# Kernel tuning notes

Measured on AMD Instinct MI355X. Metric: run time of the kernel, lower is better.

## Reference

```python
import jax, jax.numpy as jnp
import numpy as np

N = 100000   # nodes
E = 1000000  # directed edges
C = 64       # channels
K = 4        # propagation hops
DT = 1.0     # dt; exp_init=False branch: 2*x + dt^2*conv(x) - x_pre


def setup_inputs() -> dict:
    key = jax.random.key(0)
    k1, k2, k3, k4, k5 = jax.random.split(key, 5)
    x = jax.random.normal(k1, (N, C), dtype=jnp.float32)
    x_pre = jax.random.normal(k2, (N, C), dtype=jnp.float32)
    edge_index = jax.random.randint(k3, (2, E), 0, N, dtype=jnp.int32)
    bound = 1.0 / np.sqrt(C)  # PyG Linear default (kaiming-uniform-like)
    W = jax.random.uniform(k4, (C, C), jnp.float32, -bound, bound)
    b = jax.random.uniform(k5, (C,), jnp.float32, -bound, bound)
    return {"x": x, "x_pre": x_pre, "edge_index": edge_index, "W": W, "b": b}


def _sgc(x, edge_index, W, b):
    # gcn_norm: add self-loops, symmetric normalization D^-1/2 (A+I) D^-1/2
    loop = jnp.arange(N, dtype=edge_index.dtype)
    src = jnp.concatenate([edge_index[0], loop])  # source j
    dst = jnp.concatenate([edge_index[1], loop])  # target i
    deg = jax.ops.segment_sum(jnp.ones(src.shape, jnp.float32), dst, num_segments=N)
    dinv = jnp.where(deg > 0, jax.lax.rsqrt(deg), 0.0)
    norm = dinv[src] * dinv[dst]  # [E+N]
    h = x
    for _ in range(K):  # K-hop sparse propagation (gather -> scale -> scatter-add)
        h = jax.ops.segment_sum(h[src] * norm[:, None], dst, num_segments=N)
    return h @ W.T + b  # SGConv final linear


def reference(x, x_pre, edge_index, W, b):
    return 2.0 * x + (DT * DT) * _sgc(x, edge_index, W, b) - x_pre
```

## Files before the change

### kernel.cpp

```cpp
#include <hip/hip_runtime.h>
#include <hip/hip_fp16.h>

#define CCH 64
#define NBLK 128
#define BKT  256


__global__ void countA(const int* __restrict__ dst, int* __restrict__ cntmat,
                       int E, int chunk, int B) {
    __shared__ int h[512];
    int t = threadIdx.x, blk = blockIdx.x;
    for (int i = t; i < B; i += 256) h[i] = 0;
    __syncthreads();
    int e0 = blk * chunk, e1 = min(e0 + chunk, E);
    for (int e = e0 + t; e < e1; e += 256) atomicAdd(&h[dst[e] >> 8], 1);
    __syncthreads();
    for (int i = t; i < B; i += 256) cntmat[i * NBLK + blk] = h[i];
}

__global__ void scan1(const int* __restrict__ cnt, int* __restrict__ part,
                      int* __restrict__ bsum, int N) {
    __shared__ int s[256];
    int t = threadIdx.x;
    int base = blockIdx.x * 1024 + t * 4;
    int v0 = (base + 0 < N) ? cnt[base + 0] : 0;
    int v1 = (base + 1 < N) ? cnt[base + 1] : 0;
    int v2 = (base + 2 < N) ? cnt[base + 2] : 0;
    int v3 = (base + 3 < N) ? cnt[base + 3] : 0;
    s[t] = v0 + v1 + v2 + v3;
    __syncthreads();
    for (int off = 1; off < 256; off <<= 1) {
        int xx = (t >= off) ? s[t - off] : 0;
        __syncthreads();
        s[t] += xx;
        __syncthreads();
    }
    int excl = (t == 0) ? 0 : s[t - 1];
    if (t == 255) bsum[blockIdx.x] = s[255];
    if (base + 0 < N) part[base + 0] = excl;
    if (base + 1 < N) part[base + 1] = excl + v0;
    if (base + 2 < N) part[base + 2] = excl + v0 + v1;
    if (base + 3 < N) part[base + 3] = excl + v0 + v1 + v2;
}

__global__ void scan2(int* __restrict__ bsum, int NB) {
    __shared__ int s[256];
    int t = threadIdx.x;
    int base = t * 4;
    int v0 = (base + 0 < NB) ? bsum[base + 0] : 0;
    int v1 = (base + 1 < NB) ? bsum[base + 1] : 0;
    int v2 = (base + 2 < NB) ? bsum[base + 2] : 0;
    int v3 = (base + 3 < NB) ? bsum[base + 3] : 0;
    s[t] = v0 + v1 + v2 + v3;
    __syncthreads();
    for (int off = 1; off < 256; off <<= 1) {
        int xx = (t >= off) ? s[t - off] : 0;
        __syncthreads();
        s[t] += xx;
        __syncthreads();
    }
    int excl = (t == 0) ? 0 : s[t - 1];
    if (base + 0 < NB) bsum[base + 0] = excl;
    if (base + 1 < NB) bsum[base + 1] = excl + v0;
    if (base + 2 < NB) bsum[base + 2] = excl + v0 + v1;
    if (base + 3 < NB) bsum[base + 3] = excl + v0 + v1 + v2;
}

__global__ void partA(const int* __restrict__ src, const int* __restrict__ dst,
                      const int* __restrict__ part, const int* __restrict__ bsum,
                      unsigned* __restrict__ brec, int E, int chunk, int B) {
    __shared__ int cur[512];
    int t = threadIdx.x, blk = blockIdx.x;
    for (int i = t; i < B; i += 256) {
        int idx = i * NBLK + blk;
        cur[i] = part[idx] + bsum[idx >> 10];
    }
    __syncthreads();
    int e0 = blk * chunk, e1 = min(e0 + chunk, E);
    for (int e = e0 + t; e < e1; e += 256) {
        int s = src[e], d = dst[e];
        int pos = atomicAdd(&cur[d >> 8], 1);
        brec[pos] = ((unsigned)s << 8) | (unsigned)(d & 255);
    }
}

__global__ void buildB(const unsigned* __restrict__ brec, const int* __restrict__ part,
                       const int* __restrict__ bsum, int* __restrict__ row_ptr,
                       int* __restrict__ adj, float* __restrict__ dinv,
                       float* __restrict__ dinv2, const float* __restrict__ x,
                       __half* __restrict__ xh, int N, int B, int E) {
    __shared__ int hist[256];
    __shared__ int scanbuf[256];
    __shared__ int cursor[256];
    __shared__ float sdinv[256];
    int t = threadIdx.x, k = blockIdx.x;
    int i0 = k * NBLK;
    int base = part[i0] + bsum[i0 >> 10];
    int nextb;
    if (k + 1 < B) {
        int i1 = (k + 1) * NBLK;
        nextb = part[i1] + bsum[i1 >> 10];
    } else {
        nextb = E;
    }
    hist[t] = 0;
    __syncthreads();
    for (int i = base + t; i < nextb; i += 256) atomicAdd(&hist[brec[i] & 255u], 1);
    __syncthreads();
    int v = hist[t];
    scanbuf[t] = v;
    __syncthreads();
    for (int o = 1; o < 256; o <<= 1) {
        int xx = (t >= o) ? scanbuf[t - o] : 0;
        __syncthreads();
        scanbuf[t] += xx;
        __syncthreads();
    }
    int excl = scanbuf[t] - v;
    int node = k * 256 + t;
    float di = 0.f;
    if (node < N) {
        int p = base + excl;
        row_ptr[node] = p;
        cursor[t] = p;
        float dp1 = (float)v + 1.0f;
        di = rsqrtf(dp1);
        dinv[node]  = di;
        dinv2[node] = 1.0f / dp1;
    }
    sdinv[t] = di;
    if (k == 0 && t == 0) row_ptr[N] = E;
    __syncthreads();
    for (int i = base + t; i < nextb; i += 256) {
        unsigned r = brec[i];
        int pos = atomicAdd(&cursor[r & 255u], 1);
        adj[pos] = (int)(r >> 8);
    }
    int nodeBase = k * 256;
    for (int i = t; i < 2048; i += 256) {
        int nl = i >> 3;
        int node2 = nodeBase + nl;
        if (node2 < N) {
            float d = sdinv[nl];
            size_t baseE = (size_t)node2 * 64 + (size_t)(i & 7) * 8;
            float4 a = *(const float4*)&x[baseE];
            float4 c = *(const float4*)&x[baseE + 4];
            float4 o;
            __half2* op = (__half2*)&o;
            op[0] = __float22half2_rn(make_float2(d * a.x, d * a.y));
            op[1] = __float22half2_rn(make_float2(d * a.z, d * a.w));
            op[2] = __float22half2_rn(make_float2(d * c.x, d * c.y));
            op[3] = __float22half2_rn(make_float2(d * c.z, d * c.w));
            *(float4*)&xh[baseE] = o;
        }
    }
}


__device__ __forceinline__ void acc16w(float4 hv, float w, float* acc) {
    __half2* hp = (__half2*)&hv;
    #pragma unroll
    for (int i2 = 0; i2 < 4; ++i2) {
        float2 f = __half22float2(hp[i2]);
        acc[2 * i2]     = fmaf(w, f.x, acc[2 * i2]);
        acc[2 * i2 + 1] = fmaf(w, f.y, acc[2 * i2 + 1]);
    }
}

__global__ void __launch_bounds__(256, 6)
prop_kernel(const __half* __restrict__ hin, __half* __restrict__ hout,
            const int* __restrict__ row_ptr, const int* __restrict__ adj,
            const float* __restrict__ scale, int N) {
    int wid = (blockIdx.x * blockDim.x + threadIdx.x) >> 6;
    int nA = wid * 2;
    if (nA >= N) return;
    int nB = nA + 1;
    bool hasB = nB < N;
    int lane = threadIdx.x & 63;
    int grp  = lane >> 3;
    int q    = lane & 7;
    const float4* hin16 = (const float4*)hin;

    int rp0 = row_ptr[nA];
    int rp1 = row_ptr[nA + 1];
    int rp2 = hasB ? row_ptr[nA + 2] : rp1;
    int begA = rp0, cntA = rp1 - rp0;
    int begB = rp1, cntB = rp2 - rp1;
    int edA = adj[begA + lane];
    int edB = adj[begB + lane];
    float scA = scale[nA];
    float scB = hasB ? scale[nB] : 0.f;

    int selfn = (grp == 0) ? nA : ((grp == 1 && hasB) ? nB : 0);
    float4 selfv = hin16[(size_t)selfn * 8 + q];
    int nitA = cntA < 64 ? cntA : 64;
    int nitB = cntB < 64 ? cntB : 64;
    int jA0 = __shfl(edA, grp, 64);
    int jB0 = __shfl(edB, grp, 64);
    float4 pfA = hin16[(size_t)((grp < nitA) ? jA0 : 0) * 8 + q];
    float4 pfB = hin16[(size_t)((grp < nitB) ? jB0 : 0) * 8 + q];

    float accA[8] = {0.f, 0.f, 0.f, 0.f, 0.f, 0.f, 0.f, 0.f};
    float accB[8] = {0.f, 0.f, 0.f, 0.f, 0.f, 0.f, 0.f, 0.f};
    if (grp == 0)              acc16w(selfv, 1.f, accA);
    else if (grp == 1 && hasB) acc16w(selfv, 1.f, accB);

    int RA = (nitA + 7) >> 3;
    int RB = (nitB + 7) >> 3;
    int R  = RA > RB ? RA : RB;
    for (int r = 0; r < R; ++r) {
        float4 cA = pfA, cB = pfB;
        float wA = (r * 8 + grp < nitA) ? 1.f : 0.f;
        float wB = (r * 8 + grp < nitB) ? 1.f : 0.f;
        if (r + 1 < R) {
            int t1 = (r + 1) * 8 + grp;
            int jA = __shfl(edA, t1, 64);
            int jB = __shfl(edB, t1, 64);
            pfA = hin16[(size_t)((t1 < nitA) ? jA : 0) * 8 + q];
            pfB = hin16[(size_t)((t1 < nitB) ? jB : 0) * 8 + q];
        }
        acc16w(cA, wA, accA);
        acc16w(cB, wB, accB);
    }
    for (int e = begA + 64 + grp; e < begA + cntA; e += 8)
        acc16w(hin16[(size_t)adj[e] * 8 + q], 1.f, accA);
    for (int e = begB + 64 + grp; e < begB + cntB; e += 8)
        acc16w(hin16[(size_t)adj[e] * 8 + q], 1.f, accB);

    #pragma unroll
    for (int i = 0; i < 8; ++i) {
        accA[i] += __shfl_xor(accA[i], 8, 64);
        accA[i] += __shfl_xor(accA[i], 16, 64);
        accA[i] += __shfl_xor(accA[i], 32, 64);
        accB[i] += __shfl_xor(accB[i], 8, 64);
        accB[i] += __shfl_xor(accB[i], 16, 64);
        accB[i] += __shfl_xor(accB[i], 32, 64);
    }
    if (grp == 0 || (grp == 1 && hasB)) {
        int   row = (grp == 0) ? nA : nB;
        float sc  = (grp == 0) ? scA : scB;
        float v0 = (grp == 0) ? accA[0] : accB[0];
        float v1 = (grp == 0) ? accA[1] : accB[1];
        float v2 = (grp == 0) ? accA[2] : accB[2];
        float v3 = (grp == 0) ? accA[3] : accB[3];
        float v4 = (grp == 0) ? accA[4] : accB[4];
        float v5 = (grp == 0) ? accA[5] : accB[5];
        float v6 = (grp == 0) ? accA[6] : accB[6];
        float v7 = (grp == 0) ? accA[7] : accB[7];
        float4 o;
        __half2* op = (__half2*)&o;
        op[0] = __float22half2_rn(make_float2(sc * v0, sc * v1));
        op[1] = __float22half2_rn(make_float2(sc * v2, sc * v3));
        op[2] = __float22half2_rn(make_float2(sc * v4, sc * v5));
        op[3] = __float22half2_rn(make_float2(sc * v6, sc * v7));
        ((float4*)hout)[(size_t)row * 8 + q] = o;
    }
}

__global__ void __launch_bounds__(256, 2)
final_kernel(const __half* __restrict__ h, const float* __restrict__ x,
             const float* __restrict__ xp, const float* __restrict__ W,
             const float* __restrict__ b, float* __restrict__ out, int N) {
    __shared__ __align__(16) float ht[64 * 68];
    __shared__ __align__(16) float Wt[64 * 68];
    int t = threadIdx.x;
    int nodeBase = blockIdx.x * 64;

    for (int i = t; i < 1024; i += 256) {
        int c  = i >> 4;
        int k4 = i & 15;
        float4 w4 = ((const float4*)W)[i];
        Wt[(k4 * 4 + 0) * 68 + c] = w4.x;
        Wt[(k4 * 4 + 1) * 68 + c] = w4.y;
        Wt[(k4 * 4 + 2) * 68 + c] = w4.z;
        Wt[(k4 * 4 + 3) * 68 + c] = w4.w;
    }
    for (int i = t; i < 512; i += 256) {
        int n  = i >> 3;
        int k8 = i & 7;
        int node = nodeBase + n;
        float4 hv = (node < N) ? ((const float4*)h)[node * 8 + k8]
                               : make_float4(0.f, 0.f, 0.f, 0.f);
        __half2* hp = (__half2*)&hv;
        #pragma unroll
        for (int j = 0; j < 4; ++j) {
            float2 f = __half22float2(hp[j]);
            ht[(k8 * 8 + 2 * j)     * 68 + n] = f.x;
            ht[(k8 * 8 + 2 * j + 1) * 68 + n] = f.y;
        }
    }
    __syncthreads();

    int r0 = (t >> 4) * 4;
    int c0 = (t & 15) * 4;
    float acc[4][4] = {};
    #pragma unroll 8
    for (int k = 0; k < 64; ++k) {
        float4 hv = *(const float4*)&ht[k * 68 + r0];
        float4 wv = *(const float4*)&Wt[k * 68 + c0];
        acc[0][0] = fmaf(hv.x, wv.x, acc[0][0]);
        acc[0][1] = fmaf(hv.x, wv.y, acc[0][1]);
        acc[0][2] = fmaf(hv.x, wv.z, acc[0][2]);
        acc[0][3] = fmaf(hv.x, wv.w, acc[0][3]);
        acc[1][0] = fmaf(hv.y, wv.x, acc[1][0]);
        acc[1][1] = fmaf(hv.y, wv.y, acc[1][1]);
        acc[1][2] = fmaf(hv.y, wv.z, acc[1][2]);
        acc[1][3] = fmaf(hv.y, wv.w, acc[1][3]);
        acc[2][0] = fmaf(hv.z, wv.x, acc[2][0]);
        acc[2][1] = fmaf(hv.z, wv.y, acc[2][1]);
        acc[2][2] = fmaf(hv.z, wv.z, acc[2][2]);
        acc[2][3] = fmaf(hv.z, wv.w, acc[2][3]);
        acc[3][0] = fmaf(hv.w, wv.x, acc[3][0]);
        acc[3][1] = fmaf(hv.w, wv.y, acc[3][1]);
        acc[3][2] = fmaf(hv.w, wv.z, acc[3][2]);
        acc[3][3] = fmaf(hv.w, wv.w, acc[3][3]);
    }

    float4 bv = *(const float4*)&b[c0];
    #pragma unroll
    for (int i = 0; i < 4; ++i) {
        int node = nodeBase + r0 + i;
        if (node >= N) continue;
        int base = node * 64 + c0;
        float4 xv = *(const float4*)&x[base];
        float4 pv = *(const float4*)&xp[base];
        float4 o;
        o.x = fmaf(2.f, xv.x, acc[i][0] + bv.x) - pv.x;
        o.y = fmaf(2.f, xv.y, acc[i][1] + bv.y) - pv.y;
        o.z = fmaf(2.f, xv.z, acc[i][2] + bv.z) - pv.z;
        o.w = fmaf(2.f, xv.w, acc[i][3] + bv.w) - pv.w;
        *(float4*)&out[base] = o;
    }
}

extern "C" void kernel_launch(void* const* d_in, const int* in_sizes, int n_in,
                              void* d_out, int out_size, void* d_ws, size_t ws_size,
                              hipStream_t stream) {
    const float* x    = (const float*)d_in[0];
    const float* xpre = (const float*)d_in[1];
    const int*   ei   = (const int*)d_in[2];
    const float* W    = (const float*)d_in[3];
    const float* b    = (const float*)d_in[4];
    float* out = (float*)d_out;

    const int N = in_sizes[0] / CCH;
    const int E = in_sizes[2] / 2;
    const int* src = ei;
    const int* dst = ei + E;

    const int B     = (N + BKT - 1) / BKT;
    const int M     = B * NBLK;
    const int chunk = (E + NBLK - 1) / NBLK;
    const int NB2   = (M + 1023) / 1024;

    char* p = (char*)d_ws;
    auto alloc = [&](size_t bytes) -> char* {
        char* r = p;
        p += (bytes + 255) & ~(size_t)255;
        return r;
    };
    int*      cntmat  = (int*)alloc((size_t)M * 4);
    int*      part    = (int*)alloc((size_t)M * 4);
    int*      bsum    = (int*)alloc((size_t)NB2 * 4);
    unsigned* brec    = (unsigned*)alloc((size_t)E * 4);
    int*      adj     = (int*)alloc(((size_t)E + 64) * 4);
    int*      row_ptr = (int*)alloc(((size_t)N + 1) * 4);
    float*    dinv    = (float*)alloc((size_t)N * 4);
    float*    dinv2   = (float*)alloc((size_t)N * 4);
    __half*   xh      = (__half*)alloc((size_t)N * CCH * 2);
    __half*   g0      = (__half*)alloc((size_t)N * CCH * 2);
    __half*   g1      = (__half*)alloc((size_t)N * CCH * 2);

    countA<<<NBLK, 256, 0, stream>>>(dst, cntmat, E, chunk, B);
    scan1 <<<NB2, 256, 0, stream>>>(cntmat, part, bsum, M);
    scan2 <<<1, 256, 0, stream>>>(bsum, NB2);
    partA <<<NBLK, 256, 0, stream>>>(src, dst, part, bsum, brec, E, chunk, B);
    buildB<<<B, 256, 0, stream>>>(brec, part, bsum, row_ptr, adj, dinv, dinv2,
                                  x, xh, N, B, E);

    const int nw    = (N + 1) / 2;
    const int pgrid = (nw + 3) / 4;
    prop_kernel<<<pgrid, 256, 0, stream>>>(xh, g0, row_ptr, adj, dinv2, N);
    prop_kernel<<<pgrid, 256, 0, stream>>>(g0, g1, row_ptr, adj, dinv2, N);
    prop_kernel<<<pgrid, 256, 0, stream>>>(g1, g0, row_ptr, adj, dinv2, N);
    prop_kernel<<<pgrid, 256, 0, stream>>>(g0, g1, row_ptr, adj, dinv,  N);

    final_kernel<<<(N + 63) / 64, 256, 0, stream>>>(g1, x, xpre, W, b, out, N);
}
```

Before: 292.7 us.

## Remap propagation to eight nodes per wavefront with software-pipelined gathers

The SpMM propagation kernel now gives each 8-lane group its own node, so one wavefront handles eight rows instead of two. Each group walks its edge list serially with a double-buffered register pipeline of four outstanding gathers, and adjacency indices are prefetched eight at a time. This aims to raise memory-level parallelism, remove the cross-lane reduction and the 64-edge cap path, and lift occupancy to 8 waves per SIMD. In exchange, a wavefront runs for as long as its highest-degree node, so skewed degrees cause lane divergence. The adjacency buffer padding grows to cover the prefetch overrun.

```diff
diff --git a/kernel.cpp b/kernel.cpp
--- a/kernel.cpp
+++ b/kernel.cpp
@@ -167,93 +167,90 @@
     }
 }
 
-__global__ void __launch_bounds__(256, 6)
+__global__ void __launch_bounds__(256, 8)
 prop_kernel(const __half* __restrict__ hin, __half* __restrict__ hout,
             const int* __restrict__ row_ptr, const int* __restrict__ adj,
-            const float* __restrict__ scale, int N) {
-    int wid = (blockIdx.x * blockDim.x + threadIdx.x) >> 6;
-    int nA = wid * 2;
-    if (nA >= N) return;
-    int nB = nA + 1;
-    bool hasB = nB < N;
+            const float* __restrict__ scale, int N, int E) {
+    int wid  = (blockIdx.x * blockDim.x + threadIdx.x) >> 6;
     int lane = threadIdx.x & 63;
-    int grp  = lane >> 3;
+    int g    = lane >> 3;
     int q    = lane & 7;
+    int g8   = g << 3;
+    int nb   = wid << 3;
+    if (nb >= N) return;
+    int node  = nb + g;
+    int nodeC = (node < N) ? node : (N - 1);
+    int rp0 = row_ptr[nodeC];
+    int rp1 = row_ptr[nodeC + 1];
+    int cnt = (node < N) ? (rp1 - rp0) : 0;
+
+    int R = cnt;
+    R = max(R, __shfl_xor(R, 8, 64));
+    R = max(R, __shfl_xor(R, 16, 64));
+    R = max(R, __shfl_xor(R, 32, 64));
+
     const float4* hin16 = (const float4*)hin;
 
-    int rp0 = row_ptr[nA];
-    int rp1 = row_ptr[nA + 1];
-    int rp2 = hasB ? row_ptr[nA + 2] : rp1;
-    int begA = rp0, cntA = rp1 - rp0;
-    int begB = rp1, cntB = rp2 - rp1;
-    int edA = adj[begA + lane];
-    int edB = adj[begB + lane];
-    float scA = scale[nA];
-    float scB = hasB ? scale[nB] : 0.f;
-
-    int selfn = (grp == 0) ? nA : ((grp == 1 && hasB) ? nB : 0);
-    float4 selfv = hin16[(size_t)selfn * 8 + q];
-    int nitA = cntA < 64 ? cntA : 64;
-    int nitB = cntB < 64 ? cntB : 64;
-    int jA0 = __shfl(edA, grp, 64);
-    int jB0 = __shfl(edB, grp, 64);
-    float4 pfA = hin16[(size_t)((grp < nitA) ? jA0 : 0) * 8 + q];
-    float4 pfB = hin16[(size_t)((grp < nitB) ? jB0 : 0) * 8 + q];
-
-    float accA[8] = {0.f, 0.f, 0.f, 0.f, 0.f, 0.f, 0.f, 0.f};
-    float accB[8] = {0.f, 0.f, 0.f, 0.f, 0.f, 0.f, 0.f, 0.f};
-    if (grp == 0)              acc16w(selfv, 1.f, accA);
-    else if (grp == 1 && hasB) acc16w(selfv, 1.f, accB);
-
-    int RA = (nitA + 7) >> 3;
-    int RB = (nitB + 7) >> 3;
-    int R  = RA > RB ? RA : RB;
-    for (int r = 0; r < R; ++r) {
-        float4 cA = pfA, cB = pfB;
-        float wA = (r * 8 + grp < nitA) ? 1.f : 0.f;
-        float wB = (r * 8 + grp < nitB) ? 1.f : 0.f;
-        if (r + 1 < R) {
-            int t1 = (r + 1) * 8 + grp;
-            int jA = __shfl(edA, t1, 64);
-            int jB = __shfl(edB, t1, 64);
-            pfA = hin16[(size_t)((t1 < nitA) ? jA : 0) * 8 + q];
-            pfB = hin16[(size_t)((t1 < nitB) ? jB : 0) * 8 + q];
-        }
-        acc16w(cA, wA, accA);
-        acc16w(cB, wB, accB);
-    }
-    for (int e = begA + 64 + grp; e < begA + cntA; e += 8)
-        acc16w(hin16[(size_t)adj[e] * 8 + q], 1.f, accA);
-    for (int e = begB + 64 + grp; e < begB + cntB; e += 8)
-        acc16w(hin16[(size_t)adj[e] * 8 + q], 1.f, accB);
-
-    #pragma unroll
-    for (int i = 0; i < 8; ++i) {
-        accA[i] += __shfl_xor(accA[i], 8, 64);
-        accA[i] += __shfl_xor(accA[i], 16, 64);
-        accA[i] += __shfl_xor(accA[i], 32, 64);
-        accB[i] += __shfl_xor(accB[i], 8, 64);
-        accB[i] += __shfl_xor(accB[i], 16, 64);
-        accB[i] += __shfl_xor(accB[i], 32, 64);
-    }
-    if (grp == 0 || (grp == 1 && hasB)) {
-        int   row = (grp == 0) ? nA : nB;
-        float sc  = (grp == 0) ? scA : scB;
-        float v0 = (grp == 0) ? accA[0] : accB[0];
-        float v1 = (grp == 0) ? accA[1] : accB[1];
-        float v2 = (grp == 0) ? accA[2] : accB[2];
-        float v3 = (grp == 0) ? accA[3] : accB[3];
-        float v4 = (grp == 0) ? accA[4] : accB[4];
-        float v5 = (grp == 0) ? accA[5] : accB[5];
-        float v6 = (grp == 0) ? accA[6] : accB[6];
-        float v7 = (grp == 0) ? accA[7] : accB[7];
+    int eCur = adj[rp0 + q];
+    int eNxt = adj[rp0 + 8 + q];
+
+    float4 selfv = hin16[(size_t)nodeC * 8 + q];
+
+    int j0 = __shfl(eCur, g8 + 0, 64); j0 = (0 < cnt) ? j0 : 0;
+    int j1 = __shfl(eCur, g8 + 1, 64); j1 = (1 < cnt) ? j1 : 0;
+    int j2 = __shfl(eCur, g8 + 2, 64); j2 = (2 < cnt) ? j2 : 0;
+    int j3 = __shfl(eCur, g8 + 3, 64); j3 = (3 < cnt) ? j3 : 0;
+    float4 gA0 = hin16[(size_t)j0 * 8 + q];
+    float4 gA1 = hin16[(size_t)j1 * 8 + q];
+    float4 gA2 = hin16[(size_t)j2 * 8 + q];
+    float4 gA3 = hin16[(size_t)j3 * 8 + q];
+    float4 gB0, gB1, gB2, gB3;
+
+    float acc[8] = {0.f, 0.f, 0.f, 0.f, 0.f, 0.f, 0.f, 0.f};
+    acc16w(selfv, 1.f, acc);
+
+    for (int r = 0; r < R; r += 8) {
+        int t;
+        t = r + 4; j0 = __shfl(eCur, g8 + (t & 7), 64); j0 = (t < cnt) ? j0 : 0;
+        t = r + 5; j1 = __shfl(eCur, g8 + (t & 7), 64); j1 = (t < cnt) ? j1 : 0;
+        t = r + 6; j2 = __shfl(eCur, g8 + (t & 7), 64); j2 = (t < cnt) ? j2 : 0;
+        t = r + 7; j3 = __shfl(eCur, g8 + (t & 7), 64); j3 = (t < cnt) ? j3 : 0;
+        gB0 = hin16[(size_t)j0 * 8 + q];
+        gB1 = hin16[(size_t)j1 * 8 + q];
+        gB2 = hin16[(size_t)j2 * 8 + q];
+        gB3 = hin16[(size_t)j3 * 8 + q];
+        float w;
+        w = (r + 0 < cnt) ? 1.f : 0.f; acc16w(gA0, w, acc);
+        w = (r + 1 < cnt) ? 1.f : 0.f; acc16w(gA1, w, acc);
+        w = (r + 2 < cnt) ? 1.f : 0.f; acc16w(gA2, w, acc);
+        w = (r + 3 < cnt) ? 1.f : 0.f; acc16w(gA3, w, acc);
+        t = r + 8;  j0 = __shfl(eNxt, g8 + (t & 7), 64); j0 = (t < cnt) ? j0 : 0;
+        t = r + 9;  j1 = __shfl(eNxt, g8 + (t & 7), 64); j1 = (t < cnt) ? j1 : 0;
+        t = r + 10; j2 = __shfl(eNxt, g8 + (t & 7), 64); j2 = (t < cnt) ? j2 : 0;
+        t = r + 11; j3 = __shfl(eNxt, g8 + (t & 7), 64); j3 = (t < cnt) ? j3 : 0;
+        gA0 = hin16[(size_t)j0 * 8 + q];
+        gA1 = hin16[(size_t)j1 * 8 + q];
+        gA2 = hin16[(size_t)j2 * 8 + q];
+        gA3 = hin16[(size_t)j3 * 8 + q];
+        w = (r + 4 < cnt) ? 1.f : 0.f; acc16w(gB0, w, acc);
+        w = (r + 5 < cnt) ? 1.f : 0.f; acc16w(gB1, w, acc);
+        w = (r + 6 < cnt) ? 1.f : 0.f; acc16w(gB2, w, acc);
+        w = (r + 7 < cnt) ? 1.f : 0.f; acc16w(gB3, w, acc);
+        eCur = eNxt;
+        int ao = rp0 + r + 16;
+        ao = (ao > E + 96) ? (E + 96) : ao;
+        eNxt = adj[ao + q];
+    }
+
+    float sc = scale[nodeC];
+    if (node < N) {
         float4 o;
         __half2* op = (__half2*)&o;
-        op[0] = __float22half2_rn(make_float2(sc * v0, sc * v1));
-        op[1] = __float22half2_rn(make_float2(sc * v2, sc * v3));
-        op[2] = __float22half2_rn(make_float2(sc * v4, sc * v5));
-        op[3] = __float22half2_rn(make_float2(sc * v6, sc * v7));
-        ((float4*)hout)[(size_t)row * 8 + q] = o;
+        op[0] = __float22half2_rn(make_float2(sc * acc[0], sc * acc[1]));
+        op[1] = __float22half2_rn(make_float2(sc * acc[2], sc * acc[3]));
+        op[2] = __float22half2_rn(make_float2(sc * acc[4], sc * acc[5]));
+        op[3] = __float22half2_rn(make_float2(sc * acc[6], sc * acc[7]));
+        ((float4*)hout)[(size_t)node * 8 + q] = o;
     }
 }
 
@@ -363,7 +360,7 @@
     int*      part    = (int*)alloc((size_t)M * 4);
     int*      bsum    = (int*)alloc((size_t)NB2 * 4);
     unsigned* brec    = (unsigned*)alloc((size_t)E * 4);
-    int*      adj     = (int*)alloc(((size_t)E + 64) * 4);
+    int*      adj     = (int*)alloc(((size_t)E + 128) * 4);
     int*      row_ptr = (int*)alloc(((size_t)N + 1) * 4);
     float*    dinv    = (float*)alloc((size_t)N * 4);
     float*    dinv2   = (float*)alloc((size_t)N * 4);
@@ -378,12 +375,12 @@
     buildB<<<B, 256, 0, stream>>>(brec, part, bsum, row_ptr, adj, dinv, dinv2,
                                   x, xh, N, B, E);
 
-    const int nw    = (N + 1) / 2;
-    const int pgrid = (nw + 3) / 4;
-    prop_kernel<<<pgrid, 256, 0, stream>>>(xh, g0, row_ptr, adj, dinv2, N);
-    prop_kernel<<<pgrid, 256, 0, stream>>>(g0, g1, row_ptr, adj, dinv2, N);
-    prop_kernel<<<pgrid, 256, 0, stream>>>(g1, g0, row_ptr, adj, dinv2, N);
-    prop_kernel<<<pgrid, 256, 0, stream>>>(g0, g1, row_ptr, adj, dinv,  N);
+    const int nwave = (N + 7) / 8;
+    const int pgrid = (nwave + 3) / 4;
+    prop_kernel<<<pgrid, 256, 0, stream>>>(xh, g0, row_ptr, adj, dinv2, N, E);
+    prop_kernel<<<pgrid, 256, 0, stream>>>(g0, g1, row_ptr, adj, dinv2, N, E);
+    prop_kernel<<<pgrid, 256, 0, stream>>>(g1, g0, row_ptr, adj, dinv2, N, E);
+    prop_kernel<<<pgrid, 256, 0, stream>>>(g0, g1, row_ptr, adj, dinv,  N, E);
 
     final_kernel<<<(N + 63) / 64, 256, 0, stream>>>(g1, x, xpre, W, b, out, N);
 }
```

Result: faster. 264.9 us (-9.5%).
